# Kernel optimization log

Hardware: AMD Instinct MI355X
Metric: run time of the kernel (lower is better)

## Reference

```python
import jax, jax.numpy as jnp
import numpy as np

B = 2048          # batch size
L = 8192          # number of fine-grained labels
G = 256           # meta_label_size (number of label groups)
BETA = 0.01       # config.beta


def setup_inputs() -> dict:
    key = jax.random.key(0)
    k1, k2, k3 = jax.random.split(key, 3)
    logits = jax.random.normal(k1, (B, L), dtype=jnp.float32)
    true_y = jax.random.randint(k2, (B, L), 0, 2, dtype=jnp.int32)
    group_ids = jax.random.randint(k3, (L,), 0, G, dtype=jnp.int32)
    return {"logits": logits, "true_y": true_y, "group_ids": group_ids}


def reference(logits, true_y, group_ids):
    # y_hat = sigmoid(logits); meta_prob[b, g] = prod_{l in group g} (1 - y_hat[b, l])
    # Using 1 - sigmoid(x) = sigmoid(-x):
    #   log meta_prob = segment_sum(log_sigmoid(-logits)) over labels per group.
    log_not = jax.nn.log_sigmoid(-logits)                                    # [B, L]
    grp_log = jax.ops.segment_sum(log_not.T, group_ids, num_segments=G).T    # [B, G]
    meta_probs = jnp.exp(grp_log)                                            # [B, G]

    # meta_y[b, g] = 1 if any true label of group g is set in row b (generate_meta_y)
    any_true = jax.ops.segment_sum(true_y.T.astype(jnp.float32), group_ids,
                                   num_segments=G).T                         # [B, G]
    meta_y = (any_true > 0).astype(logits.dtype)

    # BCELoss (mean reduction, torch clamps log terms at -100)
    log_p = jnp.maximum(grp_log, -100.0)
    log_1mp = jnp.maximum(jnp.log1p(-meta_probs), -100.0)
    bce = -jnp.mean(meta_y * log_p + (1.0 - meta_y) * log_1mp)
    return bce * BETA
```

## Files before the change

### kernel.cpp

```cpp
#include <hip/hip_runtime.h>
#include <math.h>

constexpr int   B_    = 2048;
constexpr int   L_    = 8192;
constexpr int   G_    = 256;
constexpr float BETA_ = 0.01f;
constexpr float BIG_  = 1024.0f;

constexpr int   HALF  = L_ / 2;
constexpr int   PMAX  = HALF + G_ * 3;

__device__ __forceinline__ float log_sigmoid_neg(float x) {
    return -(fmaxf(x, 0.0f) + __logf(1.0f + __expf(-fabsf(x))));
}

extern "C" __global__ __launch_bounds__(1024)
void build_rank_kernel(const int* __restrict__ group_ids,
                       int* __restrict__ g_offs,
                       unsigned short* __restrict__ g_rank)
{
    __shared__ int s_cnt[G_];
    __shared__ int s_scan[G_];
    __shared__ int s_cur[G_];

    const int t = threadIdx.x;
    const int h = blockIdx.x;

    if (t < G_) s_cnt[t] = 0;

    const int4 ids = ((const int4*)group_ids)[h * 1024 + t];
    __syncthreads();

    atomicAdd(&s_cnt[ids.x], 1);
    atomicAdd(&s_cnt[ids.y], 1);
    atomicAdd(&s_cnt[ids.z], 1);
    atomicAdd(&s_cnt[ids.w], 1);
    __syncthreads();

    if (t < G_) s_scan[t] = (s_cnt[t] + 3) & ~3;
    __syncthreads();
    for (int off = 1; off < G_; off <<= 1) {
        int v = 0;
        if (t < G_ && t >= off) v = s_scan[t - off];
        __syncthreads();
        if (t < G_) s_scan[t] += v;
        __syncthreads();
    }

    if (t < G_) {
        const int excl = s_scan[t] - ((s_cnt[t] + 3) & ~3);
        s_cur[t] = excl;
        g_offs[h * 257 + t] = excl;
    }
    if (t == 0) g_offs[h * 257 + G_] = s_scan[G_ - 1];
    __syncthreads();

    const int l = h * HALF + t * 4;
    g_rank[l + 0] = (unsigned short)atomicAdd(&s_cur[ids.x], 1);
    g_rank[l + 1] = (unsigned short)atomicAdd(&s_cur[ids.y], 1);
    g_rank[l + 2] = (unsigned short)atomicAdd(&s_cur[ids.z], 1);
    g_rank[l + 3] = (unsigned short)atomicAdd(&s_cur[ids.w], 1);
}


extern "C" __global__ __launch_bounds__(256, 8)
void meta_loss_kernel(const float* __restrict__ logits,
                      const int*   __restrict__ true_y,
                      const int*   __restrict__ g_offs,
                      const unsigned short* __restrict__ g_rank,
                      float*       __restrict__ partial)
{
    __shared__ float s_row[PMAX];

    const int t = threadIdx.x;
    const int b = blockIdx.x >> 1;
    const int h = blockIdx.x & 1;

    const float4*  lg = (const float4*)(logits + (size_t)b * L_ + h * HALF);
    const int4*    ty = (const int4*)(true_y + (size_t)b * L_ + h * HALF);
    const ushort4* rk = (const ushort4*)(g_rank + h * HALF);
    float4* s_row4 = (float4*)s_row;

    const int o0 = g_offs[h * 257 + t];
    const int o1 = g_offs[h * 257 + t + 1];

    #pragma unroll
    for (int i = 0; i < 5; ++i) {
        const int j = i * 256 + t;
        if (j < PMAX / 4) s_row4[j] = make_float4(0.f, 0.f, 0.f, 0.f);
    }
    __syncthreads();

    #pragma unroll
    for (int i = 0; i < HALF / (4 * 256); ++i) {
        const int idx = i * 256 + t;
        const float4  x = lg[idx];
        const int4    y = ty[idx];
        const ushort4 r = rk[idx];
        s_row[r.x] = log_sigmoid_neg(x.x) + (y.x ? BIG_ : 0.0f);
        s_row[r.y] = log_sigmoid_neg(x.y) + (y.y ? BIG_ : 0.0f);
        s_row[r.z] = log_sigmoid_neg(x.z) + (y.z ? BIG_ : 0.0f);
        s_row[r.w] = log_sigmoid_neg(x.w) + (y.w ? BIG_ : 0.0f);
    }
    __syncthreads();

    float4 a4 = make_float4(0.f, 0.f, 0.f, 0.f);
    for (int j = o0; j < o1; j += 4) {
        const float4 v = *(const float4*)&s_row[j];
        a4.x += v.x; a4.y += v.y; a4.z += v.z; a4.w += v.w;
    }
    const float enc = (a4.x + a4.y) + (a4.z + a4.w);

    if (o1 > o0)
        atomicAdd(&partial[b * G_ + t], enc);
}

extern "C" __global__ __launch_bounds__(1024)
void finalize_kernel(const float* __restrict__ partial,
                     float* __restrict__ out)
{
    __shared__ float s_part[16];

    const int t   = threadIdx.x;
    const int idx = blockIdx.x * 1024 + t;

    const float enc = partial[idx];
    const int   k   = __float2int_rn(enc * (1.0f / BIG_));
    const float gl  = enc - BIG_ * (float)k;

    float term;
    if (k != 0) {
        term = fmaxf(gl, -100.0f);
    } else {
        term = fmaxf(log1pf(-__expf(gl)), -100.0f);
    }

    #pragma unroll
    for (int off = 32; off > 0; off >>= 1)
        term += __shfl_down(term, off, 64);
    if ((t & 63) == 0) s_part[t >> 6] = term;
    __syncthreads();

    if (t == 0) {
        float s = 0.0f;
        #pragma unroll
        for (int w = 0; w < 16; ++w) s += s_part[w];
        atomicAdd(out, s * (-BETA_ / ((float)B_ * (float)G_)));
    }
}

extern "C" void kernel_launch(void* const* d_in, const int* in_sizes, int n_in,
                              void* d_out, int out_size, void* d_ws, size_t ws_size,
                              hipStream_t stream) {
    const float* logits    = (const float*)d_in[0];
    const int*   true_y    = (const int*)d_in[1];
    const int*   group_ids = (const int*)d_in[2];
    float*       out       = (float*)d_out;

    float*          partial = (float*)d_ws;
    unsigned short* g_rank  = (unsigned short*)((char*)d_ws + (size_t)B_ * G_ * 4);
    int*            g_offs  = (int*)((char*)d_ws + (size_t)B_ * G_ * 4 + L_ * 2);

    hipMemsetAsync(partial, 0, (size_t)B_ * G_ * 4, stream);
    hipMemsetAsync(out, 0, sizeof(float), stream);

    build_rank_kernel<<<2, 1024, 0, stream>>>(group_ids, g_offs, g_rank);
    meta_loss_kernel<<<2 * B_, 256, 0, stream>>>(logits, true_y, g_offs, g_rank, partial);
    finalize_kernel<<<(B_ * G_) / 1024, 1024, 0, stream>>>(partial, out);
}
```

Baseline: 45.28 us.

## Process two rows per block with register prefetch of next row's loads

Each meta_loss block now handles two batch rows (r0 and r0+1024). The rank vector is loaded into registers once and reused for both rows, and the second row's logits and labels are prefetched into registers while the first row is scattered and reduced. This halves the grid, amortising the shared-memory zeroing and rank/offset loads per row and overlapping global loads with compute. In exchange it uses more registers and adds extra barriers, and the smaller grid may lower memory-level parallelism on a bandwidth-bound kernel.

Result: slower. 46.54 us (+2.8%).

```diff
diff --git a/kernel.cpp b/kernel.cpp
--- a/kernel.cpp
+++ b/kernel.cpp
@@ -62,7 +62,6 @@
     g_rank[l + 3] = (unsigned short)atomicAdd(&s_cur[ids.w], 1);
 }
 
-
 extern "C" __global__ __launch_bounds__(256, 8)
 void meta_loss_kernel(const float* __restrict__ logits,
                       const int*   __restrict__ true_y,
@@ -72,47 +71,72 @@
 {
     __shared__ float s_row[PMAX];
 
-    const int t = threadIdx.x;
-    const int b = blockIdx.x >> 1;
-    const int h = blockIdx.x & 1;
+    const int t  = threadIdx.x;
+    const int h  = blockIdx.x & 1;
+    const int r0 = blockIdx.x >> 1;
 
-    const float4*  lg = (const float4*)(logits + (size_t)b * L_ + h * HALF);
-    const int4*    ty = (const int4*)(true_y + (size_t)b * L_ + h * HALF);
     const ushort4* rk = (const ushort4*)(g_rank + h * HALF);
-    float4* s_row4 = (float4*)s_row;
+    ushort4 r[4];
+    #pragma unroll
+    for (int i = 0; i < 4; ++i) r[i] = rk[i * 256 + t];
 
     const int o0 = g_offs[h * 257 + t];
     const int o1 = g_offs[h * 257 + t + 1];
 
+    float4* s_row4 = (float4*)s_row;
     #pragma unroll
     for (int i = 0; i < 5; ++i) {
         const int j = i * 256 + t;
         if (j < PMAX / 4) s_row4[j] = make_float4(0.f, 0.f, 0.f, 0.f);
     }
-    __syncthreads();
+
+    const float4* lg0 = (const float4*)(logits + (size_t)r0 * L_ + h * HALF);
+    const int4*   ty0 = (const int4*)(true_y + (size_t)r0 * L_ + h * HALF);
+    float4 X[4];
+    int4   Y[4];
+    #pragma unroll
+    for (int i = 0; i < 4; ++i) { X[i] = lg0[i * 256 + t]; Y[i] = ty0[i * 256 + t]; }
+
+    asm volatile("s_waitcnt lgkmcnt(0)" ::: "memory");
+    __builtin_amdgcn_s_barrier();
 
     #pragma unroll
-    for (int i = 0; i < HALF / (4 * 256); ++i) {
-        const int idx = i * 256 + t;
-        const float4  x = lg[idx];
-        const int4    y = ty[idx];
-        const ushort4 r = rk[idx];
-        s_row[r.x] = log_sigmoid_neg(x.x) + (y.x ? BIG_ : 0.0f);
-        s_row[r.y] = log_sigmoid_neg(x.y) + (y.y ? BIG_ : 0.0f);
-        s_row[r.z] = log_sigmoid_neg(x.z) + (y.z ? BIG_ : 0.0f);
-        s_row[r.w] = log_sigmoid_neg(x.w) + (y.w ? BIG_ : 0.0f);
+    for (int rr = 0; rr < 2; ++rr) {
+        const int b = r0 + rr * 1024;
+
+        #pragma unroll
+        for (int i = 0; i < 4; ++i) {
+            s_row[r[i].x] = log_sigmoid_neg(X[i].x) + (Y[i].x ? BIG_ : 0.0f);
+            s_row[r[i].y] = log_sigmoid_neg(X[i].y) + (Y[i].y ? BIG_ : 0.0f);
+            s_row[r[i].z] = log_sigmoid_neg(X[i].z) + (Y[i].z ? BIG_ : 0.0f);
+            s_row[r[i].w] = log_sigmoid_neg(X[i].w) + (Y[i].w ? BIG_ : 0.0f);
+        }
+
+        if (rr == 0) {
+            const int bn = r0 + 1024;
+            const float4* lg = (const float4*)(logits + (size_t)bn * L_ + h * HALF);
+            const int4*   ty = (const int4*)(true_y + (size_t)bn * L_ + h * HALF);
+            #pragma unroll
+            for (int i = 0; i < 4; ++i) { X[i] = lg[i * 256 + t]; Y[i] = ty[i * 256 + t]; }
+        }
+
+        asm volatile("s_waitcnt lgkmcnt(0)" ::: "memory");
+        __builtin_amdgcn_s_barrier();
+
+        float4 a4 = make_float4(0.f, 0.f, 0.f, 0.f);
+        for (int j = o0; j < o1; j += 4) {
+            const float4 v = *(const float4*)&s_row[j];
+            a4.x += v.x; a4.y += v.y; a4.z += v.z; a4.w += v.w;
+        }
+        const float enc = (a4.x + a4.y) + (a4.z + a4.w);
+        if (o1 > o0)
+            atomicAdd(&partial[b * G_ + t], enc);
+
+        if (rr == 0) {
+            asm volatile("s_waitcnt lgkmcnt(0)" ::: "memory");
+            __builtin_amdgcn_s_barrier();
+        }
     }
-    __syncthreads();
-
-    float4 a4 = make_float4(0.f, 0.f, 0.f, 0.f);
-    for (int j = o0; j < o1; j += 4) {
-        const float4 v = *(const float4*)&s_row[j];
-        a4.x += v.x; a4.y += v.y; a4.z += v.z; a4.w += v.w;
-    }
-    const float enc = (a4.x + a4.y) + (a4.z + a4.w);
-
-    if (o1 > o0)
-        atomicAdd(&partial[b * G_ + t], enc);
 }
 
 extern "C" __global__ __launch_bounds__(1024)
@@ -165,6 +189,6 @@
     hipMemsetAsync(out, 0, sizeof(float), stream);
 
     build_rank_kernel<<<2, 1024, 0, stream>>>(group_ids, g_offs, g_rank);
-    meta_loss_kernel<<<2 * B_, 256, 0, stream>>>(logits, true_y, g_offs, g_rank, partial);
+    meta_loss_kernel<<<2 * B_ / 2, 256, 0, stream>>>(logits, true_y, g_offs, g_rank, partial);
     finalize_kernel<<<(B_ * G_) / 1024, 1024, 0, stream>>>(partial, out);
 }
```

## Stage logits and labels into LDS with async global_load_lds and chunked waits

Applied to the files above, without the earlier changes.

The per-row logits and true_y loads now go straight into two new shared staging buffers via the direct global-to-LDS load builtin. They are issued before the scatter buffer is zeroed. Processing then runs in four chunks, each gated by a partial vmcnt wait, so computation on early chunks overlaps the arrival of later ones. Rank indices are also loaded up front. The extra 32 KB of LDS per block lowers possible occupancy, and the launch bound drops from 8 to 4 blocks to match.

Result: slower. 47.58 us (+5.1%).

```diff
diff --git a/kernel.cpp b/kernel.cpp
--- a/kernel.cpp
+++ b/kernel.cpp
@@ -13,6 +13,13 @@
 __device__ __forceinline__ float log_sigmoid_neg(float x) {
     return -(fmaxf(x, 0.0f) + __logf(1.0f + __expf(-fabsf(x))));
 }
+
+#define GLOAD_LDS16(gp, lp)                                               \
+    __builtin_amdgcn_global_load_lds(                                     \
+        (const __attribute__((address_space(1))) unsigned int*)(gp),      \
+        (__attribute__((address_space(3))) unsigned int*)(lp), 16, 0, 0)
+
+#define WAITV(n) asm volatile("s_waitcnt vmcnt(" #n ")" ::: "memory")
 
 extern "C" __global__ __launch_bounds__(1024)
 void build_rank_kernel(const int* __restrict__ group_ids,
@@ -62,8 +69,7 @@
     g_rank[l + 3] = (unsigned short)atomicAdd(&s_cur[ids.w], 1);
 }
 
-
-extern "C" __global__ __launch_bounds__(256, 8)
+extern "C" __global__ __launch_bounds__(256, 4)
 void meta_loss_kernel(const float* __restrict__ logits,
                       const int*   __restrict__ true_y,
                       const int*   __restrict__ g_offs,
@@ -71,38 +77,59 @@
                       float*       __restrict__ partial)
 {
     __shared__ float s_row[PMAX];
+    __shared__ float s_stageL[HALF];
+    __shared__ int   s_stageY[HALF];
 
-    const int t = threadIdx.x;
-    const int b = blockIdx.x >> 1;
-    const int h = blockIdx.x & 1;
+    const int t    = threadIdx.x;
+    const int h    = blockIdx.x & 1;
+    const int b    = blockIdx.x >> 1;
+    const int w    = t >> 6;
+    const int lane = t & 63;
 
-    const float4*  lg = (const float4*)(logits + (size_t)b * L_ + h * HALF);
-    const int4*    ty = (const int4*)(true_y + (size_t)b * L_ + h * HALF);
     const ushort4* rk = (const ushort4*)(g_rank + h * HALF);
-    float4* s_row4 = (float4*)s_row;
-
+    const ushort4 r0q = rk[w * 256 +   0 + lane];
+    const ushort4 r1q = rk[w * 256 +  64 + lane];
+    const ushort4 r2q = rk[w * 256 + 128 + lane];
+    const ushort4 r3q = rk[w * 256 + 192 + lane];
     const int o0 = g_offs[h * 257 + t];
     const int o1 = g_offs[h * 257 + t + 1];
 
+    const float* lgh = logits + (size_t)b * L_ + h * HALF;
+    const int*   tyh = true_y + (size_t)b * L_ + h * HALF;
+    #pragma unroll
+    for (int c = 0; c < 4; ++c) {
+        const int base = w * 1024 + c * 256;
+        GLOAD_LDS16(lgh + base + lane * 4, s_stageL + base);
+        GLOAD_LDS16(tyh + base + lane * 4, s_stageY + base);
+    }
+
+    float4* s_row4 = (float4*)s_row;
     #pragma unroll
     for (int i = 0; i < 5; ++i) {
         const int j = i * 256 + t;
         if (j < PMAX / 4) s_row4[j] = make_float4(0.f, 0.f, 0.f, 0.f);
     }
-    __syncthreads();
+    asm volatile("s_waitcnt lgkmcnt(0)" ::: "memory");
+    __builtin_amdgcn_s_barrier();
 
-    #pragma unroll
-    for (int i = 0; i < HALF / (4 * 256); ++i) {
-        const int idx = i * 256 + t;
-        const float4  x = lg[idx];
-        const int4    y = ty[idx];
-        const ushort4 r = rk[idx];
-        s_row[r.x] = log_sigmoid_neg(x.x) + (y.x ? BIG_ : 0.0f);
-        s_row[r.y] = log_sigmoid_neg(x.y) + (y.y ? BIG_ : 0.0f);
-        s_row[r.z] = log_sigmoid_neg(x.z) + (y.z ? BIG_ : 0.0f);
-        s_row[r.w] = log_sigmoid_neg(x.w) + (y.w ? BIG_ : 0.0f);
-    }
-    __syncthreads();
+#define CHUNK(c, rq) do {                                                   \
+        const int base_ = w * 1024 + (c) * 256 + lane * 4;                  \
+        const float4 X = *(const float4*)&s_stageL[base_];                  \
+        const int4   Y = *(const int4*)&s_stageY[base_];                    \
+        s_row[rq.x] = log_sigmoid_neg(X.x) + (Y.x ? BIG_ : 0.0f);           \
+        s_row[rq.y] = log_sigmoid_neg(X.y) + (Y.y ? BIG_ : 0.0f);           \
+        s_row[rq.z] = log_sigmoid_neg(X.z) + (Y.z ? BIG_ : 0.0f);           \
+        s_row[rq.w] = log_sigmoid_neg(X.w) + (Y.w ? BIG_ : 0.0f);           \
+    } while (0)
+
+    WAITV(6); CHUNK(0, r0q);
+    WAITV(4); CHUNK(1, r1q);
+    WAITV(2); CHUNK(2, r2q);
+    WAITV(0); CHUNK(3, r3q);
+#undef CHUNK
+
+    asm volatile("s_waitcnt lgkmcnt(0)" ::: "memory");
+    __builtin_amdgcn_s_barrier();
 
     float4 a4 = make_float4(0.f, 0.f, 0.f, 0.f);
     for (int j = o0; j < o1; j += 4) {
@@ -110,7 +137,6 @@
         a4.x += v.x; a4.y += v.y; a4.z += v.z; a4.w += v.w;
     }
     const float enc = (a4.x + a4.y) + (a4.z + a4.w);
-
     if (o1 > o0)
         atomicAdd(&partial[b * G_ + t], enc);
 }
```

## Split labels into 8 segments with persistent blocks double-buffering rows via LDS DMA

Applied to the files above, without the earlier changes.

The label dimension is now split into 8 segments of 1024 instead of 2 halves, and a fixed grid of 1536 blocks loops over rows in a strided pattern. Each row's logits and true_y are fetched with global_load_lds directly into a double-buffered LDS stage, so the next row's load overlaps the current row's scatter and reduction. Rank and offset tables are loaded once per block. The cost is four times as many atomicAdds into partial, and extra barriers and LDS zeroing on every row.

New measurement: 56.00 us. 23.7% more time.

```diff
diff --git a/kernel.cpp b/kernel.cpp
--- a/kernel.cpp
+++ b/kernel.cpp
@@ -7,14 +7,25 @@
 constexpr float BETA_ = 0.01f;
 constexpr float BIG_  = 1024.0f;
 
-constexpr int   HALF  = L_ / 2;
-constexpr int   PMAX  = HALF + G_ * 3;
+constexpr int   SEG   = 1024;
+constexpr int   NSEG  = L_ / SEG;
+constexpr int   PMAXS = SEG + G_ * 3;
+constexpr int   RB_N  = 192;
 
 __device__ __forceinline__ float log_sigmoid_neg(float x) {
     return -(fmaxf(x, 0.0f) + __logf(1.0f + __expf(-fabsf(x))));
 }
 
-extern "C" __global__ __launch_bounds__(1024)
+#define GLOAD_LDS16(gp, lp)                                               \
+    __builtin_amdgcn_global_load_lds(                                     \
+        (const __attribute__((address_space(1))) unsigned int*)(gp),      \
+        (__attribute__((address_space(3))) unsigned int*)(lp), 16, 0, 0)
+
+#define WAITV(n) asm volatile("s_waitcnt vmcnt(" #n ")" ::: "memory")
+#define LDSBAR() do { asm volatile("s_waitcnt lgkmcnt(0)" ::: "memory"); \
+                      __builtin_amdgcn_s_barrier(); } while (0)
+
+extern "C" __global__ __launch_bounds__(256)
 void build_rank_kernel(const int* __restrict__ group_ids,
                        int* __restrict__ g_offs,
                        unsigned short* __restrict__ g_rank)
@@ -24,11 +35,10 @@
     __shared__ int s_cur[G_];
 
     const int t = threadIdx.x;
-    const int h = blockIdx.x;
+    const int q = blockIdx.x;
 
-    if (t < G_) s_cnt[t] = 0;
-
-    const int4 ids = ((const int4*)group_ids)[h * 1024 + t];
+    s_cnt[t] = 0;
+    const int4 ids = ((const int4*)group_ids)[q * 256 + t];
     __syncthreads();
 
     atomicAdd(&s_cnt[ids.x], 1);
@@ -37,82 +47,99 @@
     atomicAdd(&s_cnt[ids.w], 1);
     __syncthreads();
 
-    if (t < G_) s_scan[t] = (s_cnt[t] + 3) & ~3;
+    s_scan[t] = (s_cnt[t] + 3) & ~3;
     __syncthreads();
     for (int off = 1; off < G_; off <<= 1) {
         int v = 0;
-        if (t < G_ && t >= off) v = s_scan[t - off];
+        if (t >= off) v = s_scan[t - off];
         __syncthreads();
-        if (t < G_) s_scan[t] += v;
+        s_scan[t] += v;
         __syncthreads();
     }
 
-    if (t < G_) {
-        const int excl = s_scan[t] - ((s_cnt[t] + 3) & ~3);
-        s_cur[t] = excl;
-        g_offs[h * 257 + t] = excl;
-    }
-    if (t == 0) g_offs[h * 257 + G_] = s_scan[G_ - 1];
+    const int excl = s_scan[t] - ((s_cnt[t] + 3) & ~3);
+    s_cur[t] = excl;
+    g_offs[q * (G_ + 1) + t] = excl;
+    if (t == 0) g_offs[q * (G_ + 1) + G_] = s_scan[G_ - 1];
     __syncthreads();
 
-    const int l = h * HALF + t * 4;
+    const int l = q * SEG + t * 4;
     g_rank[l + 0] = (unsigned short)atomicAdd(&s_cur[ids.x], 1);
     g_rank[l + 1] = (unsigned short)atomicAdd(&s_cur[ids.y], 1);
     g_rank[l + 2] = (unsigned short)atomicAdd(&s_cur[ids.z], 1);
     g_rank[l + 3] = (unsigned short)atomicAdd(&s_cur[ids.w], 1);
 }
 
-
-extern "C" __global__ __launch_bounds__(256, 8)
+extern "C" __global__ __launch_bounds__(256, 6)
 void meta_loss_kernel(const float* __restrict__ logits,
                       const int*   __restrict__ true_y,
                       const int*   __restrict__ g_offs,
                       const unsigned short* __restrict__ g_rank,
                       float*       __restrict__ partial)
 {
-    __shared__ float s_row[PMAX];
+    __shared__ float s_row[PMAXS];
+    __shared__ float s_L[2][SEG];
+    __shared__ int   s_Y[2][SEG];
 
-    const int t = threadIdx.x;
-    const int b = blockIdx.x >> 1;
-    const int h = blockIdx.x & 1;
+    const int t    = threadIdx.x;
+    const int w    = t >> 6;
+    const int lane = t & 63;
+    const int q    = blockIdx.x & (NSEG - 1);
+    const int rb   = blockIdx.x >> 3;
 
-    const float4*  lg = (const float4*)(logits + (size_t)b * L_ + h * HALF);
-    const int4*    ty = (const int4*)(true_y + (size_t)b * L_ + h * HALF);
-    const ushort4* rk = (const ushort4*)(g_rank + h * HALF);
+    const ushort4 rq = ((const ushort4*)(g_rank + q * SEG))[t];
+    const int o0 = g_offs[q * (G_ + 1) + t];
+    const int o1 = g_offs[q * (G_ + 1) + t + 1];
+
+    const int nslab = (rb < (B_ - 10 * RB_N)) ? 11 : 10;
+
     float4* s_row4 = (float4*)s_row;
+    s_row4[t] = make_float4(0.f, 0.f, 0.f, 0.f);
+    if (t < PMAXS / 4 - 256) s_row4[256 + t] = make_float4(0.f, 0.f, 0.f, 0.f);
 
-    const int o0 = g_offs[h * 257 + t];
-    const int o1 = g_offs[h * 257 + t + 1];
+    const size_t colf = (size_t)q * SEG;
+    {
+        const float* lg = logits + (size_t)rb * L_ + colf;
+        const int*   ty = true_y + (size_t)rb * L_ + colf;
+        GLOAD_LDS16(lg + w * 256 + lane * 4, &s_L[0][w * 256]);
+        GLOAD_LDS16(ty + w * 256 + lane * 4, &s_Y[0][w * 256]);
+    }
+    LDSBAR();
 
-    #pragma unroll
-    for (int i = 0; i < 5; ++i) {
-        const int j = i * 256 + t;
-        if (j < PMAX / 4) s_row4[j] = make_float4(0.f, 0.f, 0.f, 0.f);
+    for (int k = 0; k < nslab; ++k) {
+        const int r   = rb + RB_N * k;
+        const int cur = k & 1;
+
+        if (k + 1 < nslab) {
+            const int rn = r + RB_N;
+            const float* lg = logits + (size_t)rn * L_ + colf;
+            const int*   ty = true_y + (size_t)rn * L_ + colf;
+            GLOAD_LDS16(lg + w * 256 + lane * 4, &s_L[cur ^ 1][w * 256]);
+            GLOAD_LDS16(ty + w * 256 + lane * 4, &s_Y[cur ^ 1][w * 256]);
+            WAITV(2);
+        } else {
+            WAITV(0);
+        }
+
+        const float4 X = ((const float4*)s_L[cur])[t];
+        const int4   Y = ((const int4*)s_Y[cur])[t];
+        s_row[rq.x] = log_sigmoid_neg(X.x) + (Y.x ? BIG_ : 0.0f);
+        s_row[rq.y] = log_sigmoid_neg(X.y) + (Y.y ? BIG_ : 0.0f);
+        s_row[rq.z] = log_sigmoid_neg(X.z) + (Y.z ? BIG_ : 0.0f);
+        s_row[rq.w] = log_sigmoid_neg(X.w) + (Y.w ? BIG_ : 0.0f);
+        LDSBAR();
+
+        float4 a4 = make_float4(0.f, 0.f, 0.f, 0.f);
+        for (int j = o0; j < o1; j += 4) {
+            const float4 v = *(const float4*)&s_row[j];
+            a4.x += v.x; a4.y += v.y; a4.z += v.z; a4.w += v.w;
+            *(float4*)&s_row[j] = make_float4(0.f, 0.f, 0.f, 0.f);
+        }
+        const float enc = (a4.x + a4.y) + (a4.z + a4.w);
+        if (o1 > o0)
+            atomicAdd(&partial[r * G_ + t], enc);
+        LDSBAR();
     }
-    __syncthreads();
-
-    #pragma unroll
-    for (int i = 0; i < HALF / (4 * 256); ++i) {
-        const int idx = i * 256 + t;
-        const float4  x = lg[idx];
-        const int4    y = ty[idx];
-        const ushort4 r = rk[idx];
-        s_row[r.x] = log_sigmoid_neg(x.x) + (y.x ? BIG_ : 0.0f);
-        s_row[r.y] = log_sigmoid_neg(x.y) + (y.y ? BIG_ : 0.0f);
-        s_row[r.z] = log_sigmoid_neg(x.z) + (y.z ? BIG_ : 0.0f);
-        s_row[r.w] = log_sigmoid_neg(x.w) + (y.w ? BIG_ : 0.0f);
-    }
-    __syncthreads();
-
-    float4 a4 = make_float4(0.f, 0.f, 0.f, 0.f);
-    for (int j = o0; j < o1; j += 4) {
-        const float4 v = *(const float4*)&s_row[j];
-        a4.x += v.x; a4.y += v.y; a4.z += v.z; a4.w += v.w;
-    }
-    const float enc = (a4.x + a4.y) + (a4.z + a4.w);
-
-    if (o1 > o0)
-        atomicAdd(&partial[b * G_ + t], enc);
 }
 
 extern "C" __global__ __launch_bounds__(1024)
@@ -164,7 +191,7 @@
     hipMemsetAsync(partial, 0, (size_t)B_ * G_ * 4, stream);
     hipMemsetAsync(out, 0, sizeof(float), stream);
 
-    build_rank_kernel<<<2, 1024, 0, stream>>>(group_ids, g_offs, g_rank);
-    meta_loss_kernel<<<2 * B_, 256, 0, stream>>>(logits, true_y, g_offs, g_rank, partial);
+    build_rank_kernel<<<NSEG, 256, 0, stream>>>(group_ids, g_offs, g_rank);
+    meta_loss_kernel<<<NSEG * RB_N, 256, 0, stream>>>(logits, true_y, g_offs, g_rank, partial);
     finalize_kernel<<<(B_ * G_) / 1024, 1024, 0, stream>>>(partial, out);
 }
```
